# Performance work log

Hardware: AMD Instinct MI355X
Metric: run time of the kernel (lower is better)

## Reference

```python
import jax, jax.numpy as jnp
import numpy as np

ETA = 0.01      # EMA adaptation rate
EPS = 1e-08     # numerical stability constant
BATCH, N_ASSETS = 262144, 128


def setup_inputs() -> dict:
    key = jax.random.key(0)
    k1, k2 = jax.random.split(key)
    weights = jax.random.normal(k1, (BATCH, N_ASSETS), dtype=jnp.float32)
    next_returns = jax.random.normal(k2, (BATCH, N_ASSETS), dtype=jnp.float32)
    A0 = jnp.float32(0.0)   # initial EMA of returns (module buffer A)
    B0 = jnp.float32(EPS)   # initial EMA of squared returns (module buffer B)
    return {"weights": weights, "next_returns": next_returns, "A0": A0, "B0": B0}


def reference(weights, next_returns, A0, B0):
    # portfolio return per time step: (batch,)
    R = jnp.sum(weights * next_returns, axis=1)

    def step(carry, r):
        A, Bm = carry
        dA = ETA * (r - A)
        dB = ETA * (r * r - Bm)
        var = jnp.maximum(Bm - A * A, EPS)
        D = (Bm * dA - 0.5 * A * dB) / (var ** 1.5)
        return (A + dA, Bm + dB), D

    (_, _), Ds = jax.lax.scan(step, (A0, B0), R)
    return -jnp.mean(Ds)
```

## Files before the change

kernel.cpp:

```cpp
#include <hip/hip_runtime.h>
#include <math.h>

#define BATCH     262144
#define NASSETS   128
#define TILE_ROWS 128
#define NBLK      (BATCH / TILE_ROWS)
#define SCHUNK    32
#define NSC       (BATCH / SCHUNK)
#define ETA       0.01
#define CDECAY    0.99
#define EPS       1e-8
#define LPAD      33

__device__ __forceinline__ int tpos(int c) { return (c & 31) * 256 + (c >> 5); }

__global__ __launch_bounds__(256) void k_rows(
    const float* __restrict__ W, const float* __restrict__ X,
    float* __restrict__ R, double* __restrict__ SAt, double* __restrict__ SBt) {
  __shared__ float part[TILE_ROWS * LPAD];
  const int t   = threadIdx.x;
  const int blk = blockIdx.x;
  const float4* W4 = reinterpret_cast<const float4*>(W) + (size_t)blk * 4096;
  const float4* X4 = reinterpret_cast<const float4*>(X) + (size_t)blk * 4096;

  #pragma unroll
  for (int b = 0; b < 4; ++b) {
    const int i0 = b * 1024 + t;
    float4 w0 = W4[i0];       float4 w1 = W4[i0 + 256];
    float4 w2 = W4[i0 + 512]; float4 w3 = W4[i0 + 768];
    float4 x0 = X4[i0];       float4 x1 = X4[i0 + 256];
    float4 x2 = X4[i0 + 512]; float4 x3 = X4[i0 + 768];
    const int r0 = (i0 >> 5), col = (i0 & 31);
    part[(r0 +  0) * LPAD + col] = w0.x*x0.x + w0.y*x0.y + w0.z*x0.z + w0.w*x0.w;
    part[(r0 +  8) * LPAD + col] = w1.x*x1.x + w1.y*x1.y + w1.z*x1.z + w1.w*x1.w;
    part[(r0 + 16) * LPAD + col] = w2.x*x2.x + w2.y*x2.y + w2.z*x2.z + w2.w*x2.w;
    part[(r0 + 24) * LPAD + col] = w3.x*x3.x + w3.y*x3.y + w3.z*x3.z + w3.w*x3.w;
  }
  __syncthreads();

  if (t < TILE_ROWS) {
    float sum = 0.f;
    #pragma unroll
    for (int j = 0; j < 32; ++j) sum += part[t * LPAD + j];
    R[(size_t)blk * TILE_ROWS + t] = sum;

    const int e = 31 - (t & 31);
    const double c1 = CDECAY, c2 = c1*c1, c4 = c2*c2, c8 = c4*c4, c16 = c8*c8;
    double wgt = ETA;
    if (e & 1)  wgt *= c1;
    if (e & 2)  wgt *= c2;
    if (e & 4)  wgt *= c4;
    if (e & 8)  wgt *= c8;
    if (e & 16) wgt *= c16;
    const double r = (double)sum;
    double sA = wgt * r, sB = wgt * r * r;
    sA += __shfl_xor(sA, 16, 64); sB += __shfl_xor(sB, 16, 64);
    sA += __shfl_xor(sA,  8, 64); sB += __shfl_xor(sB,  8, 64);
    sA += __shfl_xor(sA,  4, 64); sB += __shfl_xor(sB,  4, 64);
    sA += __shfl_xor(sA,  2, 64); sB += __shfl_xor(sB,  2, 64);
    sA += __shfl_xor(sA,  1, 64); sB += __shfl_xor(sB,  1, 64);
    if ((t & 31) == 0) {
      const int c = blk * 4 + (t >> 5);
      SAt[tpos(c)] = sA;
      SBt[tpos(c)] = sB;
    }
  }
}

__global__ __launch_bounds__(256) void k_scan(
    const double* __restrict__ SAt, const double* __restrict__ SBt,
    const float* __restrict__ A0p, const float* __restrict__ B0p,
    double* __restrict__ CAt, double* __restrict__ CBt,
    double* __restrict__ acc, unsigned* __restrict__ cnt) {
  const int l = threadIdx.x;
  const int lw = l & 63, w = l >> 6;
  __shared__ double wtot[4], wcar[4];

  double m = CDECAY;
  #pragma unroll
  for (int q = 0; q < 5; ++q) m = m * m;
  double g = m;
  #pragma unroll
  for (int q = 0; q < 5; ++q) g = g * g;
  double F = g;
  #pragma unroll
  for (int q = 0; q < 6; ++q) F = F * F;
  double glw = 1.0, gl = 1.0, p2 = g;
  #pragma unroll
  for (int b = 0; b < 8; ++b) {
    if (lw & (1 << b)) glw *= p2;
    if (l  & (1 << b)) gl  *= p2;
    p2 = p2 * p2;
  }

  #pragma unroll 1
  for (int arr = 0; arr < 2; ++arr) {
    const double* St = arr ? SBt : SAt;
    double*       Ct = arr ? CBt : CAt;
    const double init0 = arr ? (double)B0p[0] : (double)A0p[0];

    double y = 0.0;
    for (int i = 0; i < 32; ++i) y = m * y + St[i * 256 + l];

    double s = y, f = g;
    #pragma unroll
    for (int d = 1; d < 64; d <<= 1) {
      double u = __shfl_up(s, d, 64);
      if (lw >= d) s += f * u;
      f *= f;
    }
    if (lw == 63) wtot[w] = s;
    __syncthreads();
    if (l == 0) {
      double Wc = 0.0;
      for (int ww = 0; ww < 4; ++ww) { wcar[ww] = Wc; Wc = wtot[ww] + F * Wc; }
    }
    __syncthreads();
    double aIn = __shfl_up(s, 1, 64);
    if (lw == 0) aIn = 0.0;
    double A = aIn + wcar[w] * glw;
    double h = init0 * gl;
    for (int i = 0; i < 32; ++i) {
      Ct[i * 256 + l] = A + h;
      A = m * A + St[i * 256 + l];
      h *= m;
    }
    __syncthreads();
  }
  if (l == 0) { acc[0] = 0.0; cnt[0] = 0u; }
}

__global__ __launch_bounds__(256) void k_dsr(
    const float* __restrict__ R, const double* __restrict__ CAt,
    const double* __restrict__ CBt, double* __restrict__ acc,
    unsigned* __restrict__ cnt, float* __restrict__ out) {
  __shared__ float lr[256 * LPAD];
  const int t  = threadIdx.x;
  const int j0 = blockIdx.x * 256;
  const float* Rb = R + (size_t)j0 * SCHUNK;
  #pragma unroll
  for (int q = 0; q < 32; ++q) {
    const int fi = q * 256 + t;
    lr[((q * 8) + (t >> 5)) * LPAD + (t & 31)] = Rb[fi];
  }
  __syncthreads();

  const int c = j0 + t;
  double A = CAt[tpos(c)], B = CBt[tpos(c)];
  double sum = 0.0;
  #pragma unroll
  for (int k = 0; k < SCHUNK; ++k) {
    const double rv = (double)lr[t * LPAD + k];
    const double dA = ETA * (rv - A);
    const double dB = ETA * (rv * rv - B);
    double var = B - A * A;
    var = var > EPS ? var : EPS;
    sum += (B * dA - 0.5 * A * dB) / (var * sqrt(var));
    A += dA;
    B += dB;
  }
  sum += __shfl_xor(sum, 32, 64);
  sum += __shfl_xor(sum, 16, 64);
  sum += __shfl_xor(sum,  8, 64);
  sum += __shfl_xor(sum,  4, 64);
  sum += __shfl_xor(sum,  2, 64);
  sum += __shfl_xor(sum,  1, 64);
  __shared__ double red[4];
  const int wave = t >> 6, lane = t & 63;
  if (lane == 0) red[wave] = sum;
  __syncthreads();
  if (t == 0) {
    atomicAdd(acc, red[0] + red[1] + red[2] + red[3]);
    __threadfence();
    const unsigned old = atomicAdd(cnt, 1u);
    if (old == gridDim.x - 1) {
      const double v = atomicAdd(acc, 0.0);
      out[0] = (float)(-v / (double)BATCH);
    }
  }
}

extern "C" void kernel_launch(void* const* d_in, const int* in_sizes, int n_in,
                              void* d_out, int out_size, void* d_ws, size_t ws_size,
                              hipStream_t stream) {
  const float* W  = (const float*)d_in[0];
  const float* X  = (const float*)d_in[1];
  const float* A0 = (const float*)d_in[2];
  const float* B0 = (const float*)d_in[3];

  char* ws = (char*)d_ws;
  float*  R   = (float*)ws;
  double* SAt = (double*)(ws + (size_t)BATCH * 4);
  double* SBt = SAt + NSC;
  double* CAt = SBt + NSC;
  double* CBt = CAt + NSC;
  double* acc = CBt + NSC;
  unsigned* cnt = (unsigned*)(acc + 1);

  k_rows<<<NBLK, 256, 0, stream>>>(W, X, R, SAt, SBt);
  k_scan<<<1, 256, 0, stream>>>(SAt, SBt, A0, B0, CAt, CBt, acc, cnt);
  k_dsr<<<NSC / 256, 256, 0, stream>>>(R, CAt, CBt, acc, cnt, (float*)d_out);
}
```

Measured before the change: 59.20 us.

## Prefetch row tiles, split row reduction, parallelize scan halves, spread DSR blocks

k_rows now loads the next 1024-float4 slab into registers while the current one is reduced into shared memory. The 32-wide partial-sum reduction is split across all 256 threads in two halves. k_scan runs the A and B prefix scans at the same time in one 512-thread block instead of one after the other. k_dsr uses 128 chunks per block with half the threads idle, doubling the grid to spread the serial double-precision work across more CUs. The cost is higher register pressure and idle lanes in k_dsr.

```diff
diff --git a/kernel.cpp b/kernel.cpp
--- a/kernel.cpp
+++ b/kernel.cpp
@@ -14,34 +14,59 @@
 
 __device__ __forceinline__ int tpos(int c) { return (c & 31) * 256 + (c >> 5); }
 
+__device__ __forceinline__ float dot4(float4 a, float4 b) {
+  return a.x * b.x + a.y * b.y + a.z * b.z + a.w * b.w;
+}
+
 __global__ __launch_bounds__(256) void k_rows(
     const float* __restrict__ W, const float* __restrict__ X,
     float* __restrict__ R, double* __restrict__ SAt, double* __restrict__ SBt) {
   __shared__ float part[TILE_ROWS * LPAD];
+  __shared__ float hs[256];
   const int t   = threadIdx.x;
   const int blk = blockIdx.x;
   const float4* W4 = reinterpret_cast<const float4*>(W) + (size_t)blk * 4096;
   const float4* X4 = reinterpret_cast<const float4*>(X) + (size_t)blk * 4096;
 
+  float4 w0 = W4[t];       float4 w1 = W4[t + 256];
+  float4 w2 = W4[t + 512]; float4 w3 = W4[t + 768];
+  float4 x0 = X4[t];       float4 x1 = X4[t + 256];
+  float4 x2 = X4[t + 512]; float4 x3 = X4[t + 768];
+
   #pragma unroll
   for (int b = 0; b < 4; ++b) {
-    const int i0 = b * 1024 + t;
-    float4 w0 = W4[i0];       float4 w1 = W4[i0 + 256];
-    float4 w2 = W4[i0 + 512]; float4 w3 = W4[i0 + 768];
-    float4 x0 = X4[i0];       float4 x1 = X4[i0 + 256];
-    float4 x2 = X4[i0 + 512]; float4 x3 = X4[i0 + 768];
-    const int r0 = (i0 >> 5), col = (i0 & 31);
-    part[(r0 +  0) * LPAD + col] = w0.x*x0.x + w0.y*x0.y + w0.z*x0.z + w0.w*x0.w;
-    part[(r0 +  8) * LPAD + col] = w1.x*x1.x + w1.y*x1.y + w1.z*x1.z + w1.w*x1.w;
-    part[(r0 + 16) * LPAD + col] = w2.x*x2.x + w2.y*x2.y + w2.z*x2.z + w2.w*x2.w;
-    part[(r0 + 24) * LPAD + col] = w3.x*x3.x + w3.y*x3.y + w3.z*x3.z + w3.w*x3.w;
+    float4 nw0, nw1, nw2, nw3, nx0, nx1, nx2, nx3;
+    if (b < 3) {
+      const int i1 = (b + 1) * 1024 + t;
+      nw0 = W4[i1];       nw1 = W4[i1 + 256];
+      nw2 = W4[i1 + 512]; nw3 = W4[i1 + 768];
+      nx0 = X4[i1];       nx1 = X4[i1 + 256];
+      nx2 = X4[i1 + 512]; nx3 = X4[i1 + 768];
+    }
+    asm volatile("" ::: "memory");
+    const int rb = b * 32 + (t >> 5), col = t & 31;
+    part[(rb +  0) * LPAD + col] = dot4(w0, x0);
+    part[(rb +  8) * LPAD + col] = dot4(w1, x1);
+    part[(rb + 16) * LPAD + col] = dot4(w2, x2);
+    part[(rb + 24) * LPAD + col] = dot4(w3, x3);
+    if (b < 3) {
+      w0 = nw0; w1 = nw1; w2 = nw2; w3 = nw3;
+      x0 = nx0; x1 = nx1; x2 = nx2; x3 = nx3;
+    }
+  }
+  __syncthreads();
+
+  {
+    const int row = t & 127, h = (t >> 7) * 16;
+    float s = 0.f;
+    #pragma unroll
+    for (int j = 0; j < 16; ++j) s += part[row * LPAD + h + j];
+    hs[t] = s;
   }
   __syncthreads();
 
   if (t < TILE_ROWS) {
-    float sum = 0.f;
-    #pragma unroll
-    for (int j = 0; j < 32; ++j) sum += part[t * LPAD + j];
+    const float sum = hs[t] + hs[t + 128];
     R[(size_t)blk * TILE_ROWS + t] = sum;
 
     const int e = 31 - (t & 31);
@@ -67,14 +92,20 @@
   }
 }
 
-__global__ __launch_bounds__(256) void k_scan(
+__global__ __launch_bounds__(512) void k_scan(
     const double* __restrict__ SAt, const double* __restrict__ SBt,
     const float* __restrict__ A0p, const float* __restrict__ B0p,
     double* __restrict__ CAt, double* __restrict__ CBt,
     double* __restrict__ acc, unsigned* __restrict__ cnt) {
-  const int l = threadIdx.x;
-  const int lw = l & 63, w = l >> 6;
-  __shared__ double wtot[4], wcar[4];
+  const int t    = threadIdx.x;
+  const int half = t >> 8;
+  const int l    = t & 255;
+  const int lw   = l & 63, w = l >> 6;
+  __shared__ double wtot[8], wcar[8];
+
+  const double* St = half ? SBt : SAt;
+  double*       Ct = half ? CBt : CAt;
+  const double init0 = half ? (double)B0p[0] : (double)A0p[0];
 
   double m = CDECAY;
   #pragma unroll
@@ -93,71 +124,68 @@
     p2 = p2 * p2;
   }
 
-  #pragma unroll 1
-  for (int arr = 0; arr < 2; ++arr) {
-    const double* St = arr ? SBt : SAt;
-    double*       Ct = arr ? CBt : CAt;
-    const double init0 = arr ? (double)B0p[0] : (double)A0p[0];
-
-    double y = 0.0;
-    for (int i = 0; i < 32; ++i) y = m * y + St[i * 256 + l];
-
-    double s = y, f = g;
-    #pragma unroll
-    for (int d = 1; d < 64; d <<= 1) {
-      double u = __shfl_up(s, d, 64);
-      if (lw >= d) s += f * u;
-      f *= f;
-    }
-    if (lw == 63) wtot[w] = s;
-    __syncthreads();
-    if (l == 0) {
-      double Wc = 0.0;
-      for (int ww = 0; ww < 4; ++ww) { wcar[ww] = Wc; Wc = wtot[ww] + F * Wc; }
-    }
-    __syncthreads();
-    double aIn = __shfl_up(s, 1, 64);
-    if (lw == 0) aIn = 0.0;
-    double A = aIn + wcar[w] * glw;
-    double h = init0 * gl;
-    for (int i = 0; i < 32; ++i) {
-      Ct[i * 256 + l] = A + h;
-      A = m * A + St[i * 256 + l];
-      h *= m;
-    }
-    __syncthreads();
-  }
-  if (l == 0) { acc[0] = 0.0; cnt[0] = 0u; }
+  double y = 0.0;
+  for (int i = 0; i < 32; ++i) y = m * y + St[i * 256 + l];
+
+  double s = y, f = g;
+  #pragma unroll
+  for (int d = 1; d < 64; d <<= 1) {
+    double u = __shfl_up(s, d, 64);
+    if (lw >= d) s += f * u;
+    f *= f;
+  }
+  if (lw == 63) wtot[half * 4 + w] = s;
+  __syncthreads();
+  if (l == 0) {
+    double Wc = 0.0;
+    for (int ww = 0; ww < 4; ++ww) {
+      wcar[half * 4 + ww] = Wc;
+      Wc = wtot[half * 4 + ww] + F * Wc;
+    }
+  }
+  __syncthreads();
+  double aIn = __shfl_up(s, 1, 64);
+  if (lw == 0) aIn = 0.0;
+  double A = aIn + wcar[half * 4 + w] * glw;
+  double h = init0 * gl;
+  for (int i = 0; i < 32; ++i) {
+    Ct[i * 256 + l] = A + h;
+    A = m * A + St[i * 256 + l];
+    h *= m;
+  }
+  if (t == 0) { acc[0] = 0.0; cnt[0] = 0u; }
 }
 
 __global__ __launch_bounds__(256) void k_dsr(
     const float* __restrict__ R, const double* __restrict__ CAt,
     const double* __restrict__ CBt, double* __restrict__ acc,
     unsigned* __restrict__ cnt, float* __restrict__ out) {
-  __shared__ float lr[256 * LPAD];
+  __shared__ float lr[128 * LPAD];
   const int t  = threadIdx.x;
-  const int j0 = blockIdx.x * 256;
+  const int j0 = blockIdx.x * 128;
   const float* Rb = R + (size_t)j0 * SCHUNK;
   #pragma unroll
-  for (int q = 0; q < 32; ++q) {
+  for (int q = 0; q < 16; ++q) {
     const int fi = q * 256 + t;
     lr[((q * 8) + (t >> 5)) * LPAD + (t & 31)] = Rb[fi];
   }
   __syncthreads();
 
-  const int c = j0 + t;
-  double A = CAt[tpos(c)], B = CBt[tpos(c)];
   double sum = 0.0;
-  #pragma unroll
-  for (int k = 0; k < SCHUNK; ++k) {
-    const double rv = (double)lr[t * LPAD + k];
-    const double dA = ETA * (rv - A);
-    const double dB = ETA * (rv * rv - B);
-    double var = B - A * A;
-    var = var > EPS ? var : EPS;
-    sum += (B * dA - 0.5 * A * dB) / (var * sqrt(var));
-    A += dA;
-    B += dB;
+  if (t < 128) {
+    const int c = j0 + t;
+    double A = CAt[tpos(c)], B = CBt[tpos(c)];
+    #pragma unroll
+    for (int k = 0; k < SCHUNK; ++k) {
+      const double rv = (double)lr[t * LPAD + k];
+      const double dA = ETA * (rv - A);
+      const double dB = ETA * (rv * rv - B);
+      double var = B - A * A;
+      var = var > EPS ? var : EPS;
+      sum += (B * dA - 0.5 * A * dB) / (var * sqrt(var));
+      A += dA;
+      B += dB;
+    }
   }
   sum += __shfl_xor(sum, 32, 64);
   sum += __shfl_xor(sum, 16, 64);
@@ -198,6 +226,6 @@
   unsigned* cnt = (unsigned*)(acc + 1);
 
   k_rows<<<NBLK, 256, 0, stream>>>(W, X, R, SAt, SBt);
-  k_scan<<<1, 256, 0, stream>>>(SAt, SBt, A0, B0, CAt, CBt, acc, cnt);
-  k_dsr<<<NSC / 256, 256, 0, stream>>>(R, CAt, CBt, acc, cnt, (float*)d_out);
-}
+  k_scan<<<1, 512, 0, stream>>>(SAt, SBt, A0, B0, CAt, CBt, acc, cnt);
+  k_dsr<<<NSC / 128, 256, 0, stream>>>(R, CAt, CBt, acc, cnt, (float*)d_out);
+}
```

Result: no change. 58.97 us (-0.4%).

## Fuse scan into row kernel via last-block pattern, use float rsqrt in DSR

Applied to the files above, without the earlier changes.

The single-block scan kernel is folded into the row-reduction kernel: each block bumps a counter, and the last block to finish runs the carry scan, which removes one kernel launch. The counters are now zeroed with a memset before launch. The row loop is simplified to 16 single float4 loads per thread with an occupancy hint, and the DSR step replaces the double divide and sqrt with a float rsqrtf cubed. The float inverse lowers precision, and the loop change may cut memory-level parallelism.

```diff
diff --git a/kernel.cpp b/kernel.cpp
--- a/kernel.cpp
+++ b/kernel.cpp
@@ -14,9 +14,16 @@
 
 __device__ __forceinline__ int tpos(int c) { return (c & 31) * 256 + (c >> 5); }
 
-__global__ __launch_bounds__(256) void k_rows(
+__device__ __forceinline__ float dot4(float4 a, float4 b) {
+  return a.x * b.x + a.y * b.y + a.z * b.z + a.w * b.w;
+}
+
+__global__ __launch_bounds__(256, 8) void k_rows(
     const float* __restrict__ W, const float* __restrict__ X,
-    float* __restrict__ R, double* __restrict__ SAt, double* __restrict__ SBt) {
+    float* __restrict__ R, double* __restrict__ SAt, double* __restrict__ SBt,
+    const float* __restrict__ A0p, const float* __restrict__ B0p,
+    double* __restrict__ CAt, double* __restrict__ CBt,
+    unsigned* __restrict__ cnt2) {
   __shared__ float part[TILE_ROWS * LPAD];
   const int t   = threadIdx.x;
   const int blk = blockIdx.x;
@@ -24,17 +31,9 @@
   const float4* X4 = reinterpret_cast<const float4*>(X) + (size_t)blk * 4096;
 
   #pragma unroll
-  for (int b = 0; b < 4; ++b) {
-    const int i0 = b * 1024 + t;
-    float4 w0 = W4[i0];       float4 w1 = W4[i0 + 256];
-    float4 w2 = W4[i0 + 512]; float4 w3 = W4[i0 + 768];
-    float4 x0 = X4[i0];       float4 x1 = X4[i0 + 256];
-    float4 x2 = X4[i0 + 512]; float4 x3 = X4[i0 + 768];
-    const int r0 = (i0 >> 5), col = (i0 & 31);
-    part[(r0 +  0) * LPAD + col] = w0.x*x0.x + w0.y*x0.y + w0.z*x0.z + w0.w*x0.w;
-    part[(r0 +  8) * LPAD + col] = w1.x*x1.x + w1.y*x1.y + w1.z*x1.z + w1.w*x1.w;
-    part[(r0 + 16) * LPAD + col] = w2.x*x2.x + w2.y*x2.y + w2.z*x2.z + w2.w*x2.w;
-    part[(r0 + 24) * LPAD + col] = w3.x*x3.x + w3.y*x3.y + w3.z*x3.z + w3.w*x3.w;
+  for (int p = 0; p < 16; ++p) {
+    const int idx = p * 256 + t;
+    part[(idx >> 5) * LPAD + (idx & 31)] = dot4(W4[idx], X4[idx]);
   }
   __syncthreads();
 
@@ -65,15 +64,19 @@
       SBt[tpos(c)] = sB;
     }
   }
-}
-
-__global__ __launch_bounds__(256) void k_scan(
-    const double* __restrict__ SAt, const double* __restrict__ SBt,
-    const float* __restrict__ A0p, const float* __restrict__ B0p,
-    double* __restrict__ CAt, double* __restrict__ CBt,
-    double* __restrict__ acc, unsigned* __restrict__ cnt) {
-  const int l = threadIdx.x;
-  const int lw = l & 63, w = l >> 6;
+  __syncthreads();
+
+  __shared__ unsigned lastf;
+  if (t == 0) {
+    __threadfence();
+    lastf = atomicAdd(cnt2, 1u);
+  }
+  __syncthreads();
+  if (lastf != NBLK - 1) return;
+  if (t == 0) __threadfence();
+  __syncthreads();
+
+  const int l = t, lw = t & 63, w = t >> 6;
   __shared__ double wtot[4], wcar[4];
 
   double m = CDECAY;
@@ -127,7 +130,6 @@
     }
     __syncthreads();
   }
-  if (l == 0) { acc[0] = 0.0; cnt[0] = 0u; }
 }
 
 __global__ __launch_bounds__(256) void k_dsr(
@@ -155,7 +157,9 @@
     const double dB = ETA * (rv * rv - B);
     double var = B - A * A;
     var = var > EPS ? var : EPS;
-    sum += (B * dA - 0.5 * A * dB) / (var * sqrt(var));
+    const double num = B * dA - 0.5 * A * dB;
+    const float inv = rsqrtf((float)var);
+    sum += num * (double)(inv * inv * inv);
     A += dA;
     B += dB;
   }
@@ -195,9 +199,10 @@
   double* CAt = SBt + NSC;
   double* CBt = CAt + NSC;
   double* acc = CBt + NSC;
-  unsigned* cnt = (unsigned*)(acc + 1);
-
-  k_rows<<<NBLK, 256, 0, stream>>>(W, X, R, SAt, SBt);
-  k_scan<<<1, 256, 0, stream>>>(SAt, SBt, A0, B0, CAt, CBt, acc, cnt);
+  unsigned* cnt  = (unsigned*)(acc + 1);
+  unsigned* cnt2 = cnt + 1;
+
+  hipMemsetAsync(acc, 0, 16, stream);
+  k_rows<<<NBLK, 256, 0, stream>>>(W, X, R, SAt, SBt, A0, B0, CAt, CBt, cnt2);
   k_dsr<<<NSC / 256, 256, 0, stream>>>(R, CAt, CBt, acc, cnt, (float*)d_out);
 }
```

Measured after the change: 153.6 us. +159.4%, slower.
